# Kernel optimization log

Hardware: AMD Instinct MI355X
Metric: run time of the kernel (lower is better)

The kernel has to match this reference:

```python
import jax, jax.numpy as jnp
import numpy as np

N_NODES = 50000
DEG = 16
N_HEAD = 4
F_IN = 32
F_OUT = 32


def setup_inputs() -> dict:
    key = jax.random.key(0)
    k_h, k_w, k_fw, k_fb = jax.random.split(key, 4)
    h = jax.random.normal(k_h, (N_NODES, F_IN), dtype=jnp.float32)
    # structured edge list: each node has DEG distinct out-neighbors
    src = jnp.repeat(jnp.arange(N_NODES, dtype=jnp.int64), DEG)          # [E]
    offs = (jnp.arange(DEG, dtype=jnp.int64) + 1) * 97                   # distinct offsets
    dst = (src.reshape(N_NODES, DEG) + offs[None, :]).reshape(-1) % N_NODES
    edge_index = jnp.stack([src, dst], axis=0)                           # [2, E]
    # params (xavier-ish init for w, small fc, zero bias)
    gain = 1.414
    bound_w = gain * np.sqrt(6.0 / (F_IN + F_OUT))
    w = jax.random.uniform(k_w, (N_HEAD, F_IN, F_OUT), jnp.float32, -bound_w, bound_w)
    bound_fc = np.sqrt(1.0 / (2 * F_OUT))
    fc_w = jax.random.uniform(k_fw, (1, 2 * F_OUT), jnp.float32, -bound_fc, bound_fc)
    fc_b = jax.random.uniform(k_fb, (1,), jnp.float32, -bound_fc, bound_fc)
    bias = jnp.zeros((F_OUT,), jnp.float32)
    return {"h": h, "edge_index": edge_index, "w": w, "fc_w": fc_w, "fc_b": fc_b, "bias": bias}


def reference(h, edge_index, w, fc_w, fc_b, bias):
    n_head, f_in, f_out = w.shape
    n = h.shape[0]
    src, dst = edge_index[0], edge_index[1]
    hp = jnp.einsum('nf,hfo->hno', h, w)                  # [H, N, F_out]
    # fc([h_src || h_dst]) decomposes into two per-node projections
    w_src = fc_w[0, :f_out]                               # [F_out]
    w_dst = fc_w[0, f_out:]
    a_src = jnp.einsum('hnf,f->hn', hp, w_src)            # [H, N]
    a_dst = jnp.einsum('hnf,f->hn', hp, w_dst)
    e = a_src[:, src] + a_dst[:, dst] + fc_b[0]           # [H, E]
    e = jax.nn.leaky_relu(e, negative_slope=0.2)
    # segment softmax over each source node's neighbor set
    seg_max = jax.ops.segment_max(e.T, src, num_segments=n)   # [N, H]
    e = jnp.exp(e - seg_max.T[:, src])
    seg_sum = jax.ops.segment_sum(e.T, src, num_segments=n)   # [N, H]
    att = e / seg_sum.T[:, src]                                # [H, E]
    # aggregate: out[h, i] = sum_{j in N(i)} att * hp[h, j]  (== adj @ hp)
    msg = att[:, :, None] * hp[:, dst, :]                      # [H, E, F_out]
    agg = jax.vmap(lambda m: jax.ops.segment_sum(m, src, num_segments=n))(msg)  # [H, N, F_out]
    out = agg.mean(axis=0) + bias                              # [N, F_out]
    return out
```

## Files before the change

### kernel.cpp

```cpp
#include <hip/hip_runtime.h>

#define N_HEAD 4
#define F_IN   32
#define F_OUT  32
#define DEG    16

__device__ __forceinline__ float4 fma4(float a, float4 x, float4 acc) {
    acc.x = fmaf(a, x.x, acc.x);
    acc.y = fmaf(a, x.y, acc.y);
    acc.z = fmaf(a, x.z, acc.z);
    acc.w = fmaf(a, x.w, acc.w);
    return acc;
}

__device__ __forceinline__ float4 shflxor4(float4 v, int m) {
    float4 r;
    r.x = __shfl_xor(v.x, m, 64);
    r.y = __shfl_xor(v.y, m, 64);
    r.z = __shfl_xor(v.z, m, 64);
    r.w = __shfl_xor(v.w, m, 64);
    return r;
}

__global__ __launch_bounds__(256) void gat_proj(
    const float* __restrict__ h, const float* __restrict__ w,
    const float* __restrict__ fc_w,
    float* __restrict__ hp, float* __restrict__ asrc, float* __restrict__ adst,
    int N)
{
    __shared__ float4 wlds[N_HEAD * F_IN * F_OUT / 4];
    int t = threadIdx.x;
    const float4* w4g = (const float4*)w;
    wlds[t]       = w4g[t];
    wlds[t + 256] = w4g[t + 256];
    wlds[t + 512] = w4g[t + 512];
    wlds[t + 768] = w4g[t + 768];
    __syncthreads();

    int wid  = t >> 6;
    int lane = t & 63;
    int p    = lane >> 5;
    int sub  = lane & 31;
    int hh   = sub >> 3;
    int q    = sub & 7;
    int node0 = blockIdx.x * 32;
    int base  = node0 + wid * 8 + p * 4;

    float4 acc[4];
    #pragma unroll
    for (int m = 0; m < 4; ++m) acc[m] = make_float4(0.f, 0.f, 0.f, 0.f);

    const float4* h4 = (const float4*)h;
    #pragma unroll
    for (int c = 0; c < 8; ++c) {
        float4 wv0 = wlds[hh * 256 + (4 * c + 0) * 8 + q];
        float4 wv1 = wlds[hh * 256 + (4 * c + 1) * 8 + q];
        float4 wv2 = wlds[hh * 256 + (4 * c + 2) * 8 + q];
        float4 wv3 = wlds[hh * 256 + (4 * c + 3) * 8 + q];
        #pragma unroll
        for (int m = 0; m < 4; ++m) {
            int node = base + m;
            int nc   = node < N ? node : N - 1;
            float4 hv = h4[(size_t)nc * 8 + c];
            acc[m] = fma4(hv.x, wv0, acc[m]);
            acc[m] = fma4(hv.y, wv1, acc[m]);
            acc[m] = fma4(hv.z, wv2, acc[m]);
            acc[m] = fma4(hv.w, wv3, acc[m]);
        }
    }

    float4 fs4 = ((const float4*)fc_w)[q];
    float4 fd4 = ((const float4*)fc_w)[8 + q];
    float ps[4], pd[4];
    #pragma unroll
    for (int m = 0; m < 4; ++m) {
        ps[m] = acc[m].x * fs4.x + acc[m].y * fs4.y + acc[m].z * fs4.z + acc[m].w * fs4.w;
        pd[m] = acc[m].x * fd4.x + acc[m].y * fd4.y + acc[m].z * fd4.z + acc[m].w * fd4.w;
    }
    #pragma unroll
    for (int msk = 1; msk <= 4; msk <<= 1) {
        #pragma unroll
        for (int m = 0; m < 4; ++m) {
            ps[m] += __shfl_xor(ps[m], msk, 64);
            pd[m] += __shfl_xor(pd[m], msk, 64);
        }
    }

    float4* hp4 = (float4*)hp;
    #pragma unroll
    for (int m = 0; m < 4; ++m) {
        int node = base + m;
        if (node < N) {
            hp4[(size_t)node * 32 + hh * 8 + q] = acc[m];
            if (q == 0) {
                asrc[node * N_HEAD + hh] = ps[m];
                adst[node * N_HEAD + hh] = pd[m];
            }
        }
    }
}

__global__ __launch_bounds__(256) void gat_agg(
    const int* __restrict__ dst, const float* __restrict__ hp,
    const float* __restrict__ asrc, const float* __restrict__ adst,
    const float* __restrict__ fc_b, const float* __restrict__ bias,
    float* __restrict__ out, int N)
{
    int wave = (int)((blockIdx.x * 256 + threadIdx.x) >> 6);
    int lane = threadIdx.x & 63;
    if (wave >= N) return;
    int node = wave;
    int e2 = lane >> 5;
    int sub = lane & 31;
    int hh = sub >> 3;
    int q  = sub & 7;

    const int4* dr4 = (const int4*)(dst + (size_t)node * DEG);
    int4 d0 = dr4[0], d1 = dr4[1], d2 = dr4[2], d3 = dr4[3];
    int dk[16] = { d0.x, d0.y, d0.z, d0.w, d1.x, d1.y, d1.z, d1.w,
                   d2.x, d2.y, d2.z, d2.w, d3.x, d3.y, d3.z, d3.w };

    float as = asrc[node * N_HEAD + hh];
    float b  = fc_b[0];

    float e[16];
    #pragma unroll
    for (int k = 0; k < 16; ++k) {
        float ad = adst[dk[k] * N_HEAD + hh];
        float v  = as + ad + b;
        e[k] = v > 0.f ? v : 0.2f * v;
    }
    float mx = e[0];
    #pragma unroll
    for (int k = 1; k < 16; ++k) mx = fmaxf(mx, e[k]);
    float s = 0.f;
    #pragma unroll
    for (int k = 0; k < 16; ++k) { e[k] = __expf(e[k] - mx); s += e[k]; }
    float inv = 1.0f / s;

    float4 acc = make_float4(0.f, 0.f, 0.f, 0.f);
    const float4* hp4 = (const float4*)hp;
    #pragma unroll
    for (int i = 0; i < 8; ++i) {
        int   dki = e2 ? dk[2 * i + 1] : dk[2 * i];
        float att = (e2 ? e[2 * i + 1] : e[2 * i]) * inv;
        float4 v = hp4[(size_t)dki * 32 + hh * 8 + q];
        acc = fma4(att, v, acc);
    }

    float4 r;
    r = shflxor4(acc, 32); acc.x += r.x; acc.y += r.y; acc.z += r.z; acc.w += r.w;
    r = shflxor4(acc, 8);  acc.x += r.x; acc.y += r.y; acc.z += r.z; acc.w += r.w;
    r = shflxor4(acc, 16); acc.x += r.x; acc.y += r.y; acc.z += r.z; acc.w += r.w;

    if (lane < 8) {
        float4 b4 = ((const float4*)bias)[q];
        float4 o4;
        o4.x = 0.25f * acc.x + b4.x;
        o4.y = 0.25f * acc.y + b4.y;
        o4.z = 0.25f * acc.z + b4.z;
        o4.w = 0.25f * acc.w + b4.w;
        ((float4*)out)[(size_t)node * 8 + q] = o4;
    }
}

extern "C" void kernel_launch(void* const* d_in, const int* in_sizes, int n_in,
                              void* d_out, int out_size, void* d_ws, size_t ws_size,
                              hipStream_t stream) {
    const float* h    = (const float*)d_in[0];
    const int*   eidx = (const int*)  d_in[1];
    const float* w    = (const float*)d_in[2];
    const float* fc_w = (const float*)d_in[3];
    const float* fc_b = (const float*)d_in[4];
    const float* bias = (const float*)d_in[5];

    int N = in_sizes[0] / F_IN;
    int E = in_sizes[1] / 2;
    const int* dst = eidx + E;

    float* hp   = (float*)d_ws;
    float* asrc = hp + (size_t)N * N_HEAD * F_OUT;
    float* adst = asrc + (size_t)N * N_HEAD;
    float* out  = (float*)d_out;

    gat_proj<<<(N + 31) / 32, 256, 0, stream>>>(h, w, fc_w, hp, asrc, adst, N);
    gat_agg <<<(N + 3) / 4,   256, 0, stream>>>(dst, hp, asrc, adst, fc_b, bias, out, N);
}
```

Baseline: 111.1 us.

## Store projected features as fp16 to halve gather traffic

The projection kernel now writes the per-head projected features to the workspace as packed fp16 instead of fp32, and the aggregation kernel gathers and widens them back to float. This halves the bytes moved by the intermediate write and by the random neighbour gather, which dominate the aggregation. Two smaller changes ride along: a fast path without bounds clamping for full blocks, and the softmax normalisation applied once after accumulation instead of per edge. The price is fp16 rounding of the intermediate features, which adds error to the output.

```diff
diff --git a/kernel.cpp b/kernel.cpp
--- a/kernel.cpp
+++ b/kernel.cpp
@@ -1,9 +1,12 @@
 #include <hip/hip_runtime.h>
+#include <hip/hip_fp16.h>
 
 #define N_HEAD 4
 #define F_IN   32
 #define F_OUT  32
 #define DEG    16
+
+union H4 { ushort4 u; __half h[4]; };
 
 __device__ __forceinline__ float4 fma4(float a, float4 x, float4 acc) {
     acc.x = fmaf(a, x.x, acc.x);
@@ -25,7 +28,7 @@
 __global__ __launch_bounds__(256) void gat_proj(
     const float* __restrict__ h, const float* __restrict__ w,
     const float* __restrict__ fc_w,
-    float* __restrict__ hp, float* __restrict__ asrc, float* __restrict__ adst,
+    ushort4* __restrict__ hp, float* __restrict__ asrc, float* __restrict__ adst,
     int N)
 {
     __shared__ float4 wlds[N_HEAD * F_IN * F_OUT / 4];
@@ -45,27 +48,46 @@
     int q    = sub & 7;
     int node0 = blockIdx.x * 32;
     int base  = node0 + wid * 8 + p * 4;
+    bool full = (node0 + 32 <= N);
 
     float4 acc[4];
     #pragma unroll
     for (int m = 0; m < 4; ++m) acc[m] = make_float4(0.f, 0.f, 0.f, 0.f);
 
     const float4* h4 = (const float4*)h;
-    #pragma unroll
-    for (int c = 0; c < 8; ++c) {
-        float4 wv0 = wlds[hh * 256 + (4 * c + 0) * 8 + q];
-        float4 wv1 = wlds[hh * 256 + (4 * c + 1) * 8 + q];
-        float4 wv2 = wlds[hh * 256 + (4 * c + 2) * 8 + q];
-        float4 wv3 = wlds[hh * 256 + (4 * c + 3) * 8 + q];
+    if (full) {
         #pragma unroll
-        for (int m = 0; m < 4; ++m) {
-            int node = base + m;
-            int nc   = node < N ? node : N - 1;
-            float4 hv = h4[(size_t)nc * 8 + c];
-            acc[m] = fma4(hv.x, wv0, acc[m]);
-            acc[m] = fma4(hv.y, wv1, acc[m]);
-            acc[m] = fma4(hv.z, wv2, acc[m]);
-            acc[m] = fma4(hv.w, wv3, acc[m]);
+        for (int c = 0; c < 8; ++c) {
+            float4 wv0 = wlds[hh * 256 + (4 * c + 0) * 8 + q];
+            float4 wv1 = wlds[hh * 256 + (4 * c + 1) * 8 + q];
+            float4 wv2 = wlds[hh * 256 + (4 * c + 2) * 8 + q];
+            float4 wv3 = wlds[hh * 256 + (4 * c + 3) * 8 + q];
+            #pragma unroll
+            for (int m = 0; m < 4; ++m) {
+                float4 hv = h4[(size_t)(base + m) * 8 + c];
+                acc[m] = fma4(hv.x, wv0, acc[m]);
+                acc[m] = fma4(hv.y, wv1, acc[m]);
+                acc[m] = fma4(hv.z, wv2, acc[m]);
+                acc[m] = fma4(hv.w, wv3, acc[m]);
+            }
+        }
+    } else {
+        #pragma unroll
+        for (int c = 0; c < 8; ++c) {
+            float4 wv0 = wlds[hh * 256 + (4 * c + 0) * 8 + q];
+            float4 wv1 = wlds[hh * 256 + (4 * c + 1) * 8 + q];
+            float4 wv2 = wlds[hh * 256 + (4 * c + 2) * 8 + q];
+            float4 wv3 = wlds[hh * 256 + (4 * c + 3) * 8 + q];
+            #pragma unroll
+            for (int m = 0; m < 4; ++m) {
+                int node = base + m;
+                int nc   = node < N ? node : N - 1;
+                float4 hv = h4[(size_t)nc * 8 + c];
+                acc[m] = fma4(hv.x, wv0, acc[m]);
+                acc[m] = fma4(hv.y, wv1, acc[m]);
+                acc[m] = fma4(hv.z, wv2, acc[m]);
+                acc[m] = fma4(hv.w, wv3, acc[m]);
+            }
         }
     }
 
@@ -86,12 +108,16 @@
         }
     }
 
-    float4* hp4 = (float4*)hp;
     #pragma unroll
     for (int m = 0; m < 4; ++m) {
         int node = base + m;
-        if (node < N) {
-            hp4[(size_t)node * 32 + hh * 8 + q] = acc[m];
+        if (full || node < N) {
+            H4 pk;
+            pk.h[0] = __float2half_rn(acc[m].x);
+            pk.h[1] = __float2half_rn(acc[m].y);
+            pk.h[2] = __float2half_rn(acc[m].z);
+            pk.h[3] = __float2half_rn(acc[m].w);
+            hp[(size_t)node * 32 + hh * 8 + q] = pk.u;
             if (q == 0) {
                 asrc[node * N_HEAD + hh] = ps[m];
                 adst[node * N_HEAD + hh] = pd[m];
@@ -101,7 +127,7 @@
 }
 
 __global__ __launch_bounds__(256) void gat_agg(
-    const int* __restrict__ dst, const float* __restrict__ hp,
+    const int* __restrict__ dst, const ushort4* __restrict__ hp,
     const float* __restrict__ asrc, const float* __restrict__ adst,
     const float* __restrict__ fc_b, const float* __restrict__ bias,
     float* __restrict__ out, int N)
@@ -139,14 +165,17 @@
     float inv = 1.0f / s;
 
     float4 acc = make_float4(0.f, 0.f, 0.f, 0.f);
-    const float4* hp4 = (const float4*)hp;
     #pragma unroll
     for (int i = 0; i < 8; ++i) {
         int   dki = e2 ? dk[2 * i + 1] : dk[2 * i];
-        float att = (e2 ? e[2 * i + 1] : e[2 * i]) * inv;
-        float4 v = hp4[(size_t)dki * 32 + hh * 8 + q];
-        acc = fma4(att, v, acc);
-    }
+        float p   = e2 ? e[2 * i + 1] : e[2 * i];
+        H4 pk;
+        pk.u = hp[(size_t)dki * 32 + hh * 8 + q];
+        float4 v = make_float4(__half2float(pk.h[0]), __half2float(pk.h[1]),
+                               __half2float(pk.h[2]), __half2float(pk.h[3]));
+        acc = fma4(p, v, acc);
+    }
+    acc.x *= inv; acc.y *= inv; acc.z *= inv; acc.w *= inv;
 
     float4 r;
     r = shflxor4(acc, 32); acc.x += r.x; acc.y += r.y; acc.z += r.z; acc.w += r.w;
@@ -178,10 +207,10 @@
     int E = in_sizes[1] / 2;
     const int* dst = eidx + E;
 
-    float* hp   = (float*)d_ws;
-    float* asrc = hp + (size_t)N * N_HEAD * F_OUT;
-    float* adst = asrc + (size_t)N * N_HEAD;
-    float* out  = (float*)d_out;
+    ushort4* hp  = (ushort4*)d_ws;
+    float* asrc  = (float*)(hp + (size_t)N * 32);
+    float* adst  = asrc + (size_t)N * N_HEAD;
+    float* out   = (float*)d_out;
 
     gat_proj<<<(N + 31) / 32, 256, 0, stream>>>(h, w, fc_w, hp, asrc, adst, N);
     gat_agg <<<(N + 3) / 4,   256, 0, stream>>>(dst, hp, asrc, adst, fc_b, bias, out, N);
```

New measurement: 108.4 us. -2.4%, faster.
